# Kernel tuning notes

Hardware: AMD Instinct MI355X
Metric: run time of the kernel (lower is better)

## Reference

```python
import jax, jax.numpy as jnp
import numpy as np

N, E, G = 50000, 800000, 64
IN_C, HID, HEADS, OUT_C = 128, 64, 4, 10
NEG_SLOPE = 0.2
EPS = 1e-16


def gat_conv(x, src, dst, W, a_src, a_dst, bias, heads, out_ch):
    # x: [N, F_in]; W: [F_in, heads*out_ch]; a_*: [heads, out_ch]; bias: [heads*out_ch]
    n = x.shape[0]
    h = (x @ W).reshape(n, heads, out_ch)                     # [N, H, C]
    alpha_src = jnp.einsum('nhc,hc->nh', h, a_src)            # [N, H]
    alpha_dst = jnp.einsum('nhc,hc->nh', h, a_dst)            # [N, H]
    e = jax.nn.leaky_relu(alpha_src[src] + alpha_dst[dst], NEG_SLOPE)  # [E, H]
    # segment softmax over incoming edges of each destination node
    m = jax.ops.segment_max(e, dst, num_segments=n)
    ex = jnp.exp(e - m[dst])
    denom = jax.ops.segment_sum(ex, dst, num_segments=n)
    alpha = ex / (denom[dst] + EPS)                           # [E, H]
    msg = h[src] * alpha[:, :, None]                          # [E, H, C]
    out = jax.ops.segment_sum(msg, dst, num_segments=n)       # [N, H, C]
    return out.reshape(n, heads * out_ch) + bias


def setup_inputs() -> dict:
    key = jax.random.key(0)
    ks = jax.random.split(key, 16)
    s = 0.1
    inp = {
        'x': jax.random.normal(ks[0], (N, IN_C), dtype=jnp.float32),
        'edge_index': jax.random.randint(ks[1], (2, E), 0, N, dtype=jnp.int64)
            if jax.config.jax_enable_x64 else jax.random.randint(ks[1], (2, E), 0, N).astype(jnp.int32),
        'batch': jnp.sort(jax.random.randint(ks[2], (N,), 0, G).astype(jnp.int32)),
        'W1': s * jax.random.normal(ks[3], (IN_C, HEADS * HID), dtype=jnp.float32),
        'as1': s * jax.random.normal(ks[4], (HEADS, HID), dtype=jnp.float32),
        'ad1': s * jax.random.normal(ks[5], (HEADS, HID), dtype=jnp.float32),
        'b1': jnp.zeros((HEADS * HID,), jnp.float32),
        'W2': s * jax.random.normal(ks[6], (HEADS * HID, HEADS * HID), dtype=jnp.float32),
        'as2': s * jax.random.normal(ks[7], (HEADS, HID), dtype=jnp.float32),
        'ad2': s * jax.random.normal(ks[8], (HEADS, HID), dtype=jnp.float32),
        'b2': jnp.zeros((HEADS * HID,), jnp.float32),
        'W3': s * jax.random.normal(ks[9], (HEADS * HID, HID), dtype=jnp.float32),
        'as3': s * jax.random.normal(ks[10], (1, HID), dtype=jnp.float32),
        'ad3': s * jax.random.normal(ks[11], (1, HID), dtype=jnp.float32),
        'b3': jnp.zeros((HID,), jnp.float32),
        'Wc': s * jax.random.normal(ks[12], (HID, OUT_C), dtype=jnp.float32),
        'bc': jnp.zeros((OUT_C,), jnp.float32),
    }
    return inp


def reference(x, edge_index, batch, W1, as1, ad1, b1, W2, as2, ad2, b2,
              W3, as3, ad3, b3, Wc, bc):
    n = x.shape[0]
    loop = jnp.arange(n, dtype=edge_index.dtype)
    src = jnp.concatenate([edge_index[0], loop])  # add self-loops (PyG default)
    dst = jnp.concatenate([edge_index[1], loop])

    h = gat_conv(x, src, dst, W1, as1, ad1, b1, HEADS, HID)
    h = jax.nn.elu(h)
    h = gat_conv(h, src, dst, W2, as2, ad2, b2, HEADS, HID)
    h = jax.nn.elu(h)
    h = gat_conv(h, src, dst, W3, as3, ad3, b3, 1, HID)

    # global mean pool over graphs
    sums = jax.ops.segment_sum(h, batch, num_segments=G)            # [G, HID]
    counts = jax.ops.segment_sum(jnp.ones((n,), h.dtype), batch, num_segments=G)
    pooled = sums / jnp.maximum(counts, 1.0)[:, None]

    logits = pooled @ Wc + bc                                       # [G, OUT_C]
    return logits
```

## Files before the change

kernel.cpp:

```cpp
#include <hip/hip_runtime.h>

#define NEG_SLOPE 0.2f
#define EPSV 1e-16f

typedef unsigned short ushort_t;
typedef unsigned char uchar_t;
typedef __attribute__((ext_vector_type(8))) short bf16x8;
typedef __attribute__((ext_vector_type(4))) float f32x4;
typedef __attribute__((ext_vector_type(2))) float f32x2;

__device__ __forceinline__ ushort_t f2bf(float f) {
    union { float f; unsigned u; } v; v.f = f;
    unsigned r = v.u + 0x7FFFu + ((v.u >> 16) & 1u);
    return (ushort_t)(r >> 16);
}
__device__ __forceinline__ float bf2f(ushort_t u) {
    union { unsigned u; float f; } v; v.u = ((unsigned)u) << 16;
    return v.f;
}
__device__ __forceinline__ uchar_t f2fp8(float f) {
    int p = __builtin_amdgcn_cvt_pk_fp8_f32(f, 0.f, 0, false);
    return (uchar_t)(p & 0xff);
}

__global__ __launch_bounds__(256)
void count_kernel(const int* __restrict__ ei, int* __restrict__ deg, int E, int n) {
    int i = blockIdx.x * blockDim.x + threadIdx.x;
    int M = E + n;
    if (i >= M) return;
    int d = (i < E) ? ei[E + i] : (i - E);
    atomicAdd(&deg[d], 1);
}

__global__ __launch_bounds__(1024)
void scan1_kernel(const int* __restrict__ deg, int* __restrict__ indptr,
                  int* __restrict__ bsum, int n) {
    __shared__ int wsum[16];
    const int t = threadIdx.x;
    const int lane = t & 63;
    const int w = t >> 6;
    const int i = blockIdx.x * 1024 + t;
    int v = (i < n) ? deg[i] : 0;
    int s = v;
    #pragma unroll
    for (int off = 1; off < 64; off <<= 1) {
        int u = __shfl_up(s, off);
        if (lane >= off) s += u;
    }
    if (lane == 63) wsum[w] = s;
    __syncthreads();
    if (t < 16) {
        int ws_ = wsum[t];
        #pragma unroll
        for (int off = 1; off < 16; off <<= 1) {
            int u = __shfl_up(ws_, off);
            if (t >= off) ws_ += u;
        }
        wsum[t] = ws_;
    }
    __syncthreads();
    int woff = (w > 0) ? wsum[w - 1] : 0;
    if (i < n) indptr[i + 1] = woff + s;
    if (t == 0) bsum[blockIdx.x] = wsum[15];
}

__global__ __launch_bounds__(1024)
void scan3_kernel(int* __restrict__ indptr, int* __restrict__ cursor,
                  const int* __restrict__ bsum, int nb, int n) {
    __shared__ int boff_s;
    const int t = threadIdx.x;
    if (t < 64) {
        int v = (t < nb) ? bsum[t] : 0;
        int s = v;
        #pragma unroll
        for (int off = 1; off < 64; off <<= 1) {
            int u = __shfl_up(s, off);
            if (t >= off) s += u;
        }
        if (t == (int)blockIdx.x) boff_s = s - v;
    }
    __syncthreads();
    const int boff = boff_s;
    int i = blockIdx.x * 1024 + t;
    if (i < n) {
        int val = indptr[i + 1] + boff;
        indptr[i + 1] = val;
        cursor[i + 1] = val;
    }
    if (i == 0) { indptr[0] = 0; cursor[0] = 0; }
}

__global__ __launch_bounds__(256)
void scatter_kernel(const int* __restrict__ ei, int* __restrict__ cursor,
                    int* __restrict__ csr_src, int* __restrict__ csr_dst, int E, int n) {
    int i = blockIdx.x * blockDim.x + threadIdx.x;
    int M = E + n;
    if (i >= M) return;
    int s, d;
    if (i < E) { s = ei[i]; d = ei[E + i]; }
    else       { s = i - E; d = i - E; }
    int pos = atomicAdd(&cursor[d], 1);
    csr_src[pos] = s;
    csr_dst[pos] = d;
}

__global__ __launch_bounds__(256)
void prep_kernel(const float* __restrict__ x, ushort_t* __restrict__ xb, int nx4,
                 const float* __restrict__ W1, ushort_t* __restrict__ Wt1,
                 const float* __restrict__ W2, ushort_t* __restrict__ Wt2,
                 const float* __restrict__ W3, ushort_t* __restrict__ Wt3,
                 int K1, int* __restrict__ deg, int n) {
    long idx = (long)blockIdx.x * 256 + threadIdx.x;
    if (idx < nx4) {
        float4 v = *reinterpret_cast<const float4*>(&x[idx * 4]);
        ushort4 o;
        o.x = f2bf(v.x); o.y = f2bf(v.y); o.z = f2bf(v.z); o.w = f2bf(v.w);
        *reinterpret_cast<ushort4*>(&xb[idx * 4]) = o;
        return;
    }
    idx -= nx4;
    if (idx < (long)K1 * 256) {
        int c = (int)(idx % 256), k = (int)(idx / 256);
        Wt1[(long)c * K1 + k] = f2bf(W1[idx]);
        return;
    }
    idx -= (long)K1 * 256;
    if (idx < 256 * 256) {
        int c = (int)(idx % 256), k = (int)(idx / 256);
        Wt2[(long)c * 256 + k] = f2bf(W2[idx]);
        return;
    }
    idx -= 256 * 256;
    if (idx < 256 * 64) {
        int c = (int)(idx % 64), k = (int)(idx / 64);
        Wt3[(long)c * 256 + k] = f2bf(W3[idx]);
        return;
    }
    idx -= 256 * 64;
    if (idx < n) deg[idx] = 0;
}

template<int NC>
__global__ __launch_bounds__(256)
void mfma_gemm_alpha_kernel(const ushort_t* __restrict__ A, const ushort_t* __restrict__ Wt,
                            uchar_t* __restrict__ C,
                            const float* __restrict__ a_src, const float* __restrict__ a_dst,
                            float* __restrict__ asrc, float* __restrict__ adst,
                            int M, int K, int N, int H) {
    constexpr int TBN = NC * 64;
    constexpr int MI  = (NC == 2) ? 4 : 2;
    __shared__ ushort_t As[128][40];
    __shared__ ushort_t Ws[TBN][40];
    const int tid  = threadIdx.x;
    const int w    = tid >> 6;
    const int lane = tid & 63;
    const int l15  = lane & 15;
    const int l4   = lane >> 4;
    const int row0 = blockIdx.x * 128;
    const int col0 = blockIdx.y * TBN;
    const int rbase = (NC == 2) ? (w & 1) * 64 : w * 32;
    const int cbase = (NC == 2) ? (w >> 1) * 64 : 0;

    f32x4 acc[MI][4];
    #pragma unroll
    for (int mi = 0; mi < MI; ++mi)
        #pragma unroll
        for (int ni = 0; ni < 4; ++ni)
            acc[mi][ni] = (f32x4){0.f, 0.f, 0.f, 0.f};

    for (int k0 = 0; k0 < K; k0 += 32) {
        #pragma unroll
        for (int it = 0; it < 2; ++it) {
            int idx = tid + it * 256;
            int r = idx >> 2, seg = idx & 3;
            int gr = row0 + r;
            uint4 v = make_uint4(0u, 0u, 0u, 0u);
            if (gr < M)
                v = *reinterpret_cast<const uint4*>(&A[(long)gr * K + k0 + seg * 8]);
            *reinterpret_cast<uint4*>(&As[r][seg * 8]) = v;
        }
        #pragma unroll
        for (int it = 0; it < NC; ++it) {
            int idx = tid + it * 256;
            int r = idx >> 2, seg = idx & 3;
            uint4 v = *reinterpret_cast<const uint4*>(&Wt[(long)(col0 + r) * K + k0 + seg * 8]);
            *reinterpret_cast<uint4*>(&Ws[r][seg * 8]) = v;
        }
        __syncthreads();
        bf16x8 af[MI], bfv[4];
        #pragma unroll
        for (int mi = 0; mi < MI; ++mi)
            af[mi] = *reinterpret_cast<const bf16x8*>(&As[rbase + mi * 16 + l15][8 * l4]);
        #pragma unroll
        for (int ni = 0; ni < 4; ++ni)
            bfv[ni] = *reinterpret_cast<const bf16x8*>(&Ws[cbase + ni * 16 + l15][8 * l4]);
        #pragma unroll
        for (int mi = 0; mi < MI; ++mi)
            #pragma unroll
            for (int ni = 0; ni < 4; ++ni)
                acc[mi][ni] = __builtin_amdgcn_mfma_f32_16x16x32_bf16(
                    af[mi], bfv[ni], acc[mi][ni], 0, 0, 0);
        __syncthreads();
    }

    #pragma unroll
    for (int mi = 0; mi < MI; ++mi)
        #pragma unroll
        for (int reg = 0; reg < 4; ++reg) {
            int gr = row0 + rbase + mi * 16 + l4 * 4 + reg;
            if (gr < M) {
                #pragma unroll
                for (int ni = 0; ni < 4; ++ni)
                    C[(long)gr * N + col0 + cbase + ni * 16 + l15] = f2fp8(acc[mi][ni][reg]);
            }
        }

    const int hd = (col0 + cbase) >> 6;
    float aS[4], aD[4];
    #pragma unroll
    for (int ni = 0; ni < 4; ++ni) {
        aS[ni] = a_src[hd * 64 + ni * 16 + l15];
        aD[ni] = a_dst[hd * 64 + ni * 16 + l15];
    }
    #pragma unroll
    for (int mi = 0; mi < MI; ++mi)
        #pragma unroll
        for (int reg = 0; reg < 4; ++reg) {
            float s = 0.f, d = 0.f;
            #pragma unroll
            for (int ni = 0; ni < 4; ++ni) {
                s += acc[mi][ni][reg] * aS[ni];
                d += acc[mi][ni][reg] * aD[ni];
            }
            #pragma unroll
            for (int off = 1; off < 16; off <<= 1) {
                s += __shfl_xor(s, off);
                d += __shfl_xor(d, off);
            }
            int gr = row0 + rbase + mi * 16 + l4 * 4 + reg;
            if (l15 == 0 && gr < M) {
                asrc[gr * H + hd] = s;
                adst[gr * H + hd] = d;
            }
        }
}

__global__ __launch_bounds__(256)
void edgeexp4_kernel(const int* __restrict__ csr_src, const int* __restrict__ csr_dst,
                     const float4* __restrict__ asrc4, const float4* __restrict__ adst4,
                     float4* __restrict__ ex4, int M) {
    int i = blockIdx.x * blockDim.x + threadIdx.x;
    if (i >= M) return;
    int s = csr_src[i], d = csr_dst[i];
    float4 a = asrc4[s];
    float4 b = adst4[d];
    float ex_, ey_, ez_, ew_;
    float e;
    e = a.x + b.x; e = e > 0.f ? e : NEG_SLOPE * e; ex_ = __expf(e);
    e = a.y + b.y; e = e > 0.f ? e : NEG_SLOPE * e; ey_ = __expf(e);
    e = a.z + b.z; e = e > 0.f ? e : NEG_SLOPE * e; ez_ = __expf(e);
    e = a.w + b.w; e = e > 0.f ? e : NEG_SLOPE * e; ew_ = __expf(e);
    ex4[i] = make_float4(ex_, ey_, ez_, ew_);
}

__global__ __launch_bounds__(256)
void edgeexp1_kernel(const int* __restrict__ csr_src, const int* __restrict__ csr_dst,
                     const float* __restrict__ asrc, const float* __restrict__ adst,
                     float* __restrict__ ex1, int M) {
    int i = blockIdx.x * blockDim.x + threadIdx.x;
    if (i >= M) return;
    float e = asrc[csr_src[i]] + adst[csr_dst[i]];
    e = e > 0.f ? e : NEG_SLOPE * e;
    ex1[i] = __expf(e);
}

__global__ __launch_bounds__(256)
void aggregate4_kernel(const uchar_t* __restrict__ h, const float* __restrict__ ex4,
                       const int* __restrict__ indptr, const int* __restrict__ csr_src,
                       const float* __restrict__ bias, ushort_t* __restrict__ out,
                       int n, int apply_elu) {
    const int node = (blockIdx.x * blockDim.x + threadIdx.x) >> 6;
    const int lane = threadIdx.x & 63;
    if (node >= n) return;
    const int hd  = lane >> 4;
    const int beg = indptr[node], end = indptr[node + 1];
    const int cnt = end - beg;
    const uchar_t* __restrict__ hrow = h + 4 * lane;
    const float* __restrict__ exh = ex4 + 4 * (long)beg + hd;

    float sum_ex = 0.f;
    float ax = 0.f, ay = 0.f, az = 0.f, aw = 0.f;
    int i = 0;
    for (; i + 8 <= cnt; i += 8) {
        int s[8];
        float ee[8];
        unsigned v[8];
        #pragma unroll
        for (int u = 0; u < 8; ++u) s[u] = csr_src[beg + i + u];
        #pragma unroll
        for (int u = 0; u < 8; ++u) ee[u] = exh[(long)(i + u) * 4];
        #pragma unroll
        for (int u = 0; u < 8; ++u)
            v[u] = *reinterpret_cast<const unsigned*>(hrow + ((long)s[u] << 8));
        #pragma unroll
        for (int u = 0; u < 8; ++u) {
            f32x2 lo = __builtin_amdgcn_cvt_pk_f32_fp8((int)v[u], false);
            f32x2 hi = __builtin_amdgcn_cvt_pk_f32_fp8((int)v[u], true);
            sum_ex += ee[u];
            ax += ee[u] * lo[0];
            ay += ee[u] * lo[1];
            az += ee[u] * hi[0];
            aw += ee[u] * hi[1];
        }
    }
    for (; i < cnt; ++i) {
        int s = csr_src[beg + i];
        float ee = exh[(long)i * 4];
        unsigned v = *reinterpret_cast<const unsigned*>(hrow + ((long)s << 8));
        f32x2 lo = __builtin_amdgcn_cvt_pk_f32_fp8((int)v, false);
        f32x2 hi = __builtin_amdgcn_cvt_pk_f32_fp8((int)v, true);
        sum_ex += ee;
        ax += ee * lo[0]; ay += ee * lo[1];
        az += ee * hi[0]; aw += ee * hi[1];
    }
    const float inv = 1.f / (sum_ex + EPSV);
    float4 b4 = *reinterpret_cast<const float4*>(bias + 4 * lane);
    float ox = ax * inv + b4.x;
    float oy = ay * inv + b4.y;
    float oz = az * inv + b4.z;
    float ow = aw * inv + b4.w;
    if (apply_elu) {
        ox = ox > 0.f ? ox : expm1f(ox);
        oy = oy > 0.f ? oy : expm1f(oy);
        oz = oz > 0.f ? oz : expm1f(oz);
        ow = ow > 0.f ? ow : expm1f(ow);
    }
    ushort4 o4;
    o4.x = f2bf(ox); o4.y = f2bf(oy); o4.z = f2bf(oz); o4.w = f2bf(ow);
    *reinterpret_cast<ushort4*>(out + (long)node * 256 + 4 * lane) = o4;
}

__global__ __launch_bounds__(256)
void aggregate_kernel(const uchar_t* __restrict__ h, const float* __restrict__ ex1,
                      const int* __restrict__ indptr, const int* __restrict__ csr_src,
                      const float* __restrict__ bias, ushort_t* __restrict__ out,
                      int n, int apply_elu) {
    const int node = (blockIdx.x * blockDim.x + threadIdx.x) >> 6;
    const int lane = threadIdx.x & 63;
    if (node >= n) return;
    const int beg = indptr[node], end = indptr[node + 1];
    const int cnt = end - beg;
    const uchar_t* __restrict__ hh = h + lane;

    float sum_ex = 0.f, acc = 0.f;
    int i = 0;
    for (; i + 8 <= cnt; i += 8) {
        int s[8];
        float ee[8];
        uchar_t b[8];
        #pragma unroll
        for (int u = 0; u < 8; ++u) s[u] = csr_src[beg + i + u];
        #pragma unroll
        for (int u = 0; u < 8; ++u) ee[u] = ex1[beg + i + u];
        #pragma unroll
        for (int u = 0; u < 8; ++u) b[u] = hh[(long)s[u] << 6];
        #pragma unroll
        for (int u = 0; u < 8; ++u) {
            f32x2 r = __builtin_amdgcn_cvt_pk_f32_fp8((int)b[u], false);
            sum_ex += ee[u];
            acc += ee[u] * r[0];
        }
    }
    for (; i < cnt; ++i) {
        int s = csr_src[beg + i];
        float ee = ex1[beg + i];
        f32x2 r = __builtin_amdgcn_cvt_pk_f32_fp8((int)hh[(long)s << 6], false);
        sum_ex += ee;
        acc += ee * r[0];
    }
    float o = acc / (sum_ex + EPSV) + bias[lane];
    if (apply_elu) o = o > 0.f ? o : expm1f(o);
    out[(long)node * 64 + lane] = f2bf(o);
}

constexpr int POOL_CHUNK = 128;

__global__ __launch_bounds__(64)
void pool_kernel(const ushort_t* __restrict__ h, const int* __restrict__ batch,
                 float* __restrict__ sums, int* __restrict__ counts, int n) {
    int lane = threadIdx.x;
    int start = blockIdx.x * POOL_CHUNK;
    if (start >= n) return;
    int end = min(start + POOL_CHUNK, n);
    int gcur = batch[start];
    float acc = 0.f;
    int run = 0;
    for (int i = start; i < end; ++i) {
        int g = batch[i];
        if (g != gcur) {
            atomicAdd(&sums[gcur * 64 + lane], acc);
            if (lane == 0) atomicAdd(&counts[gcur], run);
            acc = 0.f; run = 0; gcur = g;
        }
        acc += bf2f(h[(long)i * 64 + lane]);
        ++run;
    }
    atomicAdd(&sums[gcur * 64 + lane], acc);
    if (lane == 0) atomicAdd(&counts[gcur], run);
}

__global__ void classify_kernel(const float* __restrict__ sums, const int* __restrict__ counts,
                                const float* __restrict__ Wc, const float* __restrict__ bc,
                                float* __restrict__ out, int G) {
    int t = threadIdx.x;
    if (t >= G * 10) return;
    int g = t / 10, o = t - g * 10;
    int c_ = counts[g];
    float inv = 1.f / (float)(c_ > 1 ? c_ : 1);
    float acc = bc[o];
    for (int c = 0; c < 64; ++c)
        acc += sums[g * 64 + c] * inv * Wc[c * 10 + o];
    out[t] = acc;
}

extern "C" void kernel_launch(void* const* d_in, const int* in_sizes, int n_in,
                              void* d_out, int out_size, void* d_ws, size_t ws_size,
                              hipStream_t stream) {
    const float* x   = (const float*)d_in[0];
    const int*   ei  = (const int*)d_in[1];
    const int*   bat = (const int*)d_in[2];
    const float* W1  = (const float*)d_in[3];
    const float* as1 = (const float*)d_in[4];
    const float* ad1 = (const float*)d_in[5];
    const float* b1  = (const float*)d_in[6];
    const float* W2  = (const float*)d_in[7];
    const float* as2 = (const float*)d_in[8];
    const float* ad2 = (const float*)d_in[9];
    const float* b2  = (const float*)d_in[10];
    const float* W3  = (const float*)d_in[11];
    const float* as3 = (const float*)d_in[12];
    const float* ad3 = (const float*)d_in[13];
    const float* b3  = (const float*)d_in[14];
    const float* Wc  = (const float*)d_in[15];
    const float* bc  = (const float*)d_in[16];
    float* out = (float*)d_out;

    const int N = in_sizes[2];
    const int E = in_sizes[1] / 2;
    const int M = E + N;
    const int IN_C = in_sizes[0] / N;
    const int G = out_size / 10;

    char* p = (char*)d_ws;
    auto carve = [&](size_t bytes) -> void* {
        void* r = (void*)p;
        p += (bytes + 255) & ~(size_t)255;
        return r;
    };
    uchar_t*  hA  = (uchar_t*)carve((size_t)N * 256);
    ushort_t* hB  = (ushort_t*)carve((size_t)N * 256 * 2);
    size_t xb_ex_bytes = (size_t)M * 16;
    size_t xb_need = (size_t)N * IN_C * 2;
    if (xb_need > xb_ex_bytes) xb_ex_bytes = xb_need;
    ushort_t* xb  = (ushort_t*)carve(xb_ex_bytes);
    float*    ex  = (float*)xb;
    ushort_t* Wt1 = (ushort_t*)carve((size_t)256 * IN_C * 2);
    ushort_t* Wt2 = (ushort_t*)carve((size_t)256 * 256 * 2);
    ushort_t* Wt3 = (ushort_t*)carve((size_t)64 * 256 * 2);
    float* asrc = (float*)carve((size_t)N * 4 * 4);
    float* adst = (float*)carve((size_t)N * 4 * 4);
    float* sums = (float*)carve((size_t)G * 64 * 4 + (size_t)G * 4);
    int*   cnts = (int*)(sums + (size_t)G * 64);
    int*   deg  = (int*)carve((size_t)N * 4);
    int*   iptr = (int*)carve((size_t)(N + 1) * 4);
    int*   csr  = (int*)carve((size_t)M * 4);
    int*   csrd = (int*)carve((size_t)M * 4);
    int*   bsum = (int*)carve(256 * 4);
    (void)ws_size; (void)n_in;

    const int NB = (N + 1023) / 1024;
    const int MB = (M + 255) / 256;
    const int AGB = (N + 3) / 4;

    {
        long nx4 = (long)N * IN_C / 4;
        long total = nx4 + (long)IN_C * 256 + 256 * 256 + 256 * 64 + N;
        prep_kernel<<<(int)((total + 255) / 256), 256, 0, stream>>>(
            x, xb, (int)nx4, W1, Wt1, W2, Wt2, W3, Wt3, IN_C, deg, N);
    }

    count_kernel<<<MB, 256, 0, stream>>>(ei, deg, E, N);
    scan1_kernel<<<NB, 1024, 0, stream>>>(deg, iptr, bsum, N);
    scan3_kernel<<<NB, 1024, 0, stream>>>(iptr, deg, bsum, NB, N);
    scatter_kernel<<<MB, 256, 0, stream>>>(ei, deg, csr, csrd, E, N);

    {
        dim3 grid((N + 127) / 128, 2);
        mfma_gemm_alpha_kernel<2><<<grid, 256, 0, stream>>>(xb, Wt1, hA, as1, ad1,
                                                            asrc, adst, N, IN_C, 256, 4);
    }
    edgeexp4_kernel<<<MB, 256, 0, stream>>>(csr, csrd, (const float4*)asrc,
                                            (const float4*)adst, (float4*)ex, M);
    aggregate4_kernel<<<AGB, 256, 0, stream>>>(hA, ex, iptr, csr, b1, hB, N, 1);

    {
        dim3 grid((N + 127) / 128, 2);
        mfma_gemm_alpha_kernel<2><<<grid, 256, 0, stream>>>(hB, Wt2, hA, as2, ad2,
                                                            asrc, adst, N, 256, 256, 4);
    }
    edgeexp4_kernel<<<MB, 256, 0, stream>>>(csr, csrd, (const float4*)asrc,
                                            (const float4*)adst, (float4*)ex, M);
    aggregate4_kernel<<<AGB, 256, 0, stream>>>(hA, ex, iptr, csr, b2, hB, N, 1);

    {
        dim3 grid((N + 127) / 128, 1);
        mfma_gemm_alpha_kernel<1><<<grid, 256, 0, stream>>>(hB, Wt3, hA, as3, ad3,
                                                            asrc, adst, N, 256, 64, 1);
    }
    edgeexp1_kernel<<<MB, 256, 0, stream>>>(csr, csrd, asrc, adst, ex, M);
    aggregate_kernel<<<AGB, 256, 0, stream>>>(hA, ex, iptr, csr, b3, hB, N, 0);

    hipMemsetAsync(sums, 0, (size_t)G * 64 * 4 + (size_t)G * 4, stream);
    pool_kernel<<<(N + POOL_CHUNK - 1) / POOL_CHUNK, 64, 0, stream>>>(hB, bat, sums, cnts, N);
    classify_kernel<<<1, 640, 0, stream>>>(sums, cnts, Wc, bc, out, G);
}
```

Measured before the change: 454.2 us.

## Drop CSR dst array, make edge-exp kernels node-centric, fold pool zeroing into prep

The edge-exp kernels now walk the CSR per destination node, one wavefront per node, with the adst value loaded once. This removes the stored csr_dst array and its writes in scatter and reads in three edge passes. The pool accumulator memset is folded into the prep kernel, saving one launch. The cost is load imbalance across nodes of different degree, and idle lanes when degree is low (about 17 edges per node here, so 16-lane groups per head often run a second, mostly empty iteration).

```diff
diff --git a/kernel.cpp b/kernel.cpp
--- a/kernel.cpp
+++ b/kernel.cpp
@@ -92,7 +92,7 @@
 
 __global__ __launch_bounds__(256)
 void scatter_kernel(const int* __restrict__ ei, int* __restrict__ cursor,
-                    int* __restrict__ csr_src, int* __restrict__ csr_dst, int E, int n) {
+                    int* __restrict__ csr_src, int E, int n) {
     int i = blockIdx.x * blockDim.x + threadIdx.x;
     int M = E + n;
     if (i >= M) return;
@@ -101,7 +101,6 @@
     else       { s = i - E; d = i - E; }
     int pos = atomicAdd(&cursor[d], 1);
     csr_src[pos] = s;
-    csr_dst[pos] = d;
 }
 
 __global__ __launch_bounds__(256)
@@ -109,7 +108,8 @@
                  const float* __restrict__ W1, ushort_t* __restrict__ Wt1,
                  const float* __restrict__ W2, ushort_t* __restrict__ Wt2,
                  const float* __restrict__ W3, ushort_t* __restrict__ Wt3,
-                 int K1, int* __restrict__ deg, int n) {
+                 int K1, int* __restrict__ deg, int n,
+                 int* __restrict__ poolz, int gz) {
     long idx = (long)blockIdx.x * 256 + threadIdx.x;
     if (idx < nx4) {
         float4 v = *reinterpret_cast<const float4*>(&x[idx * 4]);
@@ -137,7 +137,9 @@
         return;
     }
     idx -= 256 * 64;
-    if (idx < n) deg[idx] = 0;
+    if (idx < n) { deg[idx] = 0; return; }
+    idx -= n;
+    if (idx < gz) poolz[idx] = 0;
 }
 
 template<int NC>
@@ -246,32 +248,38 @@
 }
 
 __global__ __launch_bounds__(256)
-void edgeexp4_kernel(const int* __restrict__ csr_src, const int* __restrict__ csr_dst,
-                     const float4* __restrict__ asrc4, const float4* __restrict__ adst4,
-                     float4* __restrict__ ex4, int M) {
-    int i = blockIdx.x * blockDim.x + threadIdx.x;
-    if (i >= M) return;
-    int s = csr_src[i], d = csr_dst[i];
-    float4 a = asrc4[s];
-    float4 b = adst4[d];
-    float ex_, ey_, ez_, ew_;
-    float e;
-    e = a.x + b.x; e = e > 0.f ? e : NEG_SLOPE * e; ex_ = __expf(e);
-    e = a.y + b.y; e = e > 0.f ? e : NEG_SLOPE * e; ey_ = __expf(e);
-    e = a.z + b.z; e = e > 0.f ? e : NEG_SLOPE * e; ez_ = __expf(e);
-    e = a.w + b.w; e = e > 0.f ? e : NEG_SLOPE * e; ew_ = __expf(e);
-    ex4[i] = make_float4(ex_, ey_, ez_, ew_);
-}
-
-__global__ __launch_bounds__(256)
-void edgeexp1_kernel(const int* __restrict__ csr_src, const int* __restrict__ csr_dst,
+void edgeexp4_kernel(const int* __restrict__ indptr, const int* __restrict__ csr_src,
                      const float* __restrict__ asrc, const float* __restrict__ adst,
-                     float* __restrict__ ex1, int M) {
-    int i = blockIdx.x * blockDim.x + threadIdx.x;
-    if (i >= M) return;
-    float e = asrc[csr_src[i]] + adst[csr_dst[i]];
-    e = e > 0.f ? e : NEG_SLOPE * e;
-    ex1[i] = __expf(e);
+                     float* __restrict__ ex4, int n) {
+    const int node = (blockIdx.x * blockDim.x + threadIdx.x) >> 6;
+    const int lane = threadIdx.x & 63;
+    if (node >= n) return;
+    const int hd = lane >> 4;
+    const int eidx = lane & 15;
+    const int beg = indptr[node], end = indptr[node + 1];
+    const float ad = adst[node * 4 + hd];
+    for (int i = beg + eidx; i < end; i += 16) {
+        int s = csr_src[i];
+        float e = asrc[s * 4 + hd] + ad;
+        e = e > 0.f ? e : NEG_SLOPE * e;
+        ex4[(long)i * 4 + hd] = __expf(e);
+    }
+}
+
+__global__ __launch_bounds__(256)
+void edgeexp1_kernel(const int* __restrict__ indptr, const int* __restrict__ csr_src,
+                     const float* __restrict__ asrc, const float* __restrict__ adst,
+                     float* __restrict__ ex1, int n) {
+    const int node = (blockIdx.x * blockDim.x + threadIdx.x) >> 6;
+    const int lane = threadIdx.x & 63;
+    if (node >= n) return;
+    const int beg = indptr[node], end = indptr[node + 1];
+    const float ad = adst[node];
+    for (int i = beg + lane; i < end; i += 64) {
+        float e = asrc[csr_src[i]] + ad;
+        e = e > 0.f ? e : NEG_SLOPE * e;
+        ex1[i] = __expf(e);
+    }
 }
 
 __global__ __launch_bounds__(256)
@@ -474,7 +482,6 @@
     int*   deg  = (int*)carve((size_t)N * 4);
     int*   iptr = (int*)carve((size_t)(N + 1) * 4);
     int*   csr  = (int*)carve((size_t)M * 4);
-    int*   csrd = (int*)carve((size_t)M * 4);
     int*   bsum = (int*)carve(256 * 4);
     (void)ws_size; (void)n_in;
 
@@ -484,23 +491,23 @@
 
     {
         long nx4 = (long)N * IN_C / 4;
-        long total = nx4 + (long)IN_C * 256 + 256 * 256 + 256 * 64 + N;
+        int gz = G * 65;
+        long total = nx4 + (long)IN_C * 256 + 256 * 256 + 256 * 64 + N + gz;
         prep_kernel<<<(int)((total + 255) / 256), 256, 0, stream>>>(
-            x, xb, (int)nx4, W1, Wt1, W2, Wt2, W3, Wt3, IN_C, deg, N);
+            x, xb, (int)nx4, W1, Wt1, W2, Wt2, W3, Wt3, IN_C, deg, N, (int*)sums, gz);
     }
 
     count_kernel<<<MB, 256, 0, stream>>>(ei, deg, E, N);
     scan1_kernel<<<NB, 1024, 0, stream>>>(deg, iptr, bsum, N);
     scan3_kernel<<<NB, 1024, 0, stream>>>(iptr, deg, bsum, NB, N);
-    scatter_kernel<<<MB, 256, 0, stream>>>(ei, deg, csr, csrd, E, N);
+    scatter_kernel<<<MB, 256, 0, stream>>>(ei, deg, csr, E, N);
 
     {
         dim3 grid((N + 127) / 128, 2);
         mfma_gemm_alpha_kernel<2><<<grid, 256, 0, stream>>>(xb, Wt1, hA, as1, ad1,
                                                             asrc, adst, N, IN_C, 256, 4);
     }
-    edgeexp4_kernel<<<MB, 256, 0, stream>>>(csr, csrd, (const float4*)asrc,
-                                            (const float4*)adst, (float4*)ex, M);
+    edgeexp4_kernel<<<AGB, 256, 0, stream>>>(iptr, csr, asrc, adst, ex, N);
     aggregate4_kernel<<<AGB, 256, 0, stream>>>(hA, ex, iptr, csr, b1, hB, N, 1);
 
     {
@@ -508,8 +515,7 @@
         mfma_gemm_alpha_kernel<2><<<grid, 256, 0, stream>>>(hB, Wt2, hA, as2, ad2,
                                                             asrc, adst, N, 256, 256, 4);
     }
-    edgeexp4_kernel<<<MB, 256, 0, stream>>>(csr, csrd, (const float4*)asrc,
-                                            (const float4*)adst, (float4*)ex, M);
+    edgeexp4_kernel<<<AGB, 256, 0, stream>>>(iptr, csr, asrc, adst, ex, N);
     aggregate4_kernel<<<AGB, 256, 0, stream>>>(hA, ex, iptr, csr, b2, hB, N, 1);
 
     {
@@ -517,10 +523,9 @@
         mfma_gemm_alpha_kernel<1><<<grid, 256, 0, stream>>>(hB, Wt3, hA, as3, ad3,
                                                             asrc, adst, N, 256, 64, 1);
     }
-    edgeexp1_kernel<<<MB, 256, 0, stream>>>(csr, csrd, asrc, adst, ex, M);
+    edgeexp1_kernel<<<AGB, 256, 0, stream>>>(iptr, csr, asrc, adst, ex, N);
     aggregate_kernel<<<AGB, 256, 0, stream>>>(hA, ex, iptr, csr, b3, hB, N, 0);
 
-    hipMemsetAsync(sums, 0, (size_t)G * 64 * 4 + (size_t)G * 4, stream);
     pool_kernel<<<(N + POOL_CHUNK - 1) / POOL_CHUNK, 64, 0, stream>>>(hB, bat, sums, cnts, N);
     classify_kernel<<<1, 640, 0, stream>>>(sums, cnts, Wc, bc, out, G);
 }
```

Result: slower. 473.6 us (+4.3%).

## Replicate degree counters and pack CSR src/dst into 16-bit pairs

Applied to the files above, without the earlier changes.

Degree counting and scatter use 8 replicated counter arrays selected by block index to spread atomic contention, with the scan computing per-replica cursor offsets. The CSR source and destination are packed into one 32-bit word (16 bits each), halving index reads in the edge kernels. The pool-sum memset is folded into the prep kernel. Packing assumes node count fits in 16 bits and the replicas add scan work and memory.

```diff
diff --git a/kernel.cpp b/kernel.cpp
--- a/kernel.cpp
+++ b/kernel.cpp
@@ -24,23 +24,27 @@
 }
 
 __global__ __launch_bounds__(256)
-void count_kernel(const int* __restrict__ ei, int* __restrict__ deg, int E, int n) {
+void count_kernel(const int* __restrict__ ei, int* __restrict__ deg8, int E, int n) {
     int i = blockIdx.x * blockDim.x + threadIdx.x;
     int M = E + n;
     if (i >= M) return;
     int d = (i < E) ? ei[E + i] : (i - E);
-    atomicAdd(&deg[d], 1);
+    atomicAdd(&deg8[(blockIdx.x & 7) * n + d], 1);
 }
 
 __global__ __launch_bounds__(1024)
-void scan1_kernel(const int* __restrict__ deg, int* __restrict__ indptr,
+void scan1_kernel(const int* __restrict__ deg8, int* __restrict__ indptr,
                   int* __restrict__ bsum, int n) {
     __shared__ int wsum[16];
     const int t = threadIdx.x;
     const int lane = t & 63;
     const int w = t >> 6;
     const int i = blockIdx.x * 1024 + t;
-    int v = (i < n) ? deg[i] : 0;
+    int v = 0;
+    if (i < n) {
+        #pragma unroll
+        for (int j = 0; j < 8; ++j) v += deg8[j * n + i];
+    }
     int s = v;
     #pragma unroll
     for (int off = 1; off < 64; off <<= 1) {
@@ -65,10 +69,13 @@
 }
 
 __global__ __launch_bounds__(1024)
-void scan3_kernel(int* __restrict__ indptr, int* __restrict__ cursor,
+void scan3_kernel(int* __restrict__ indptr, int* __restrict__ deg8,
                   const int* __restrict__ bsum, int nb, int n) {
     __shared__ int boff_s;
     const int t = threadIdx.x;
+    const int i = blockIdx.x * 1024 + t;
+    int lv1 = (i < n) ? indptr[i + 1] : 0;
+    int lv0 = (i < n && t > 0) ? indptr[i] : 0;
     if (t < 64) {
         int v = (t < nb) ? bsum[t] : 0;
         int s = v;
@@ -81,27 +88,30 @@
     }
     __syncthreads();
     const int boff = boff_s;
-    int i = blockIdx.x * 1024 + t;
     if (i < n) {
-        int val = indptr[i + 1] + boff;
-        indptr[i + 1] = val;
-        cursor[i + 1] = val;
-    }
-    if (i == 0) { indptr[0] = 0; cursor[0] = 0; }
-}
-
-__global__ __launch_bounds__(256)
-void scatter_kernel(const int* __restrict__ ei, int* __restrict__ cursor,
-                    int* __restrict__ csr_src, int* __restrict__ csr_dst, int E, int n) {
+        indptr[i + 1] = lv1 + boff;
+        int running = (t == 0) ? boff : lv0 + boff;
+        #pragma unroll
+        for (int j = 0; j < 8; ++j) {
+            int c = deg8[j * n + i];
+            deg8[j * n + i] = running;
+            running += c;
+        }
+    }
+    if (i == 0) indptr[0] = 0;
+}
+
+__global__ __launch_bounds__(256)
+void scatter_kernel(const int* __restrict__ ei, int* __restrict__ cursor8,
+                    unsigned* __restrict__ csrp, int E, int n) {
     int i = blockIdx.x * blockDim.x + threadIdx.x;
     int M = E + n;
     if (i >= M) return;
     int s, d;
     if (i < E) { s = ei[i]; d = ei[E + i]; }
     else       { s = i - E; d = i - E; }
-    int pos = atomicAdd(&cursor[d], 1);
-    csr_src[pos] = s;
-    csr_dst[pos] = d;
+    int pos = atomicAdd(&cursor8[(blockIdx.x & 7) * n + d], 1);
+    csrp[pos] = (unsigned)s | ((unsigned)d << 16);
 }
 
 __global__ __launch_bounds__(256)
@@ -109,7 +119,8 @@
                  const float* __restrict__ W1, ushort_t* __restrict__ Wt1,
                  const float* __restrict__ W2, ushort_t* __restrict__ Wt2,
                  const float* __restrict__ W3, ushort_t* __restrict__ Wt3,
-                 int K1, int* __restrict__ deg, int n) {
+                 int K1, int* __restrict__ deg8, int n8,
+                 int* __restrict__ poolz, int gz) {
     long idx = (long)blockIdx.x * 256 + threadIdx.x;
     if (idx < nx4) {
         float4 v = *reinterpret_cast<const float4*>(&x[idx * 4]);
@@ -137,7 +148,9 @@
         return;
     }
     idx -= 256 * 64;
-    if (idx < n) deg[idx] = 0;
+    if (idx < n8) { deg8[idx] = 0; return; }
+    idx -= n8;
+    if (idx < gz) poolz[idx] = 0;
 }
 
 template<int NC>
@@ -246,16 +259,16 @@
 }
 
 __global__ __launch_bounds__(256)
-void edgeexp4_kernel(const int* __restrict__ csr_src, const int* __restrict__ csr_dst,
+void edgeexp4_kernel(const unsigned* __restrict__ csrp,
                      const float4* __restrict__ asrc4, const float4* __restrict__ adst4,
                      float4* __restrict__ ex4, int M) {
     int i = blockIdx.x * blockDim.x + threadIdx.x;
     if (i >= M) return;
-    int s = csr_src[i], d = csr_dst[i];
+    unsigned v = csrp[i];
+    int s = (int)(v & 0xffffu), d = (int)(v >> 16);
     float4 a = asrc4[s];
     float4 b = adst4[d];
-    float ex_, ey_, ez_, ew_;
-    float e;
+    float e, ex_, ey_, ez_, ew_;
     e = a.x + b.x; e = e > 0.f ? e : NEG_SLOPE * e; ex_ = __expf(e);
     e = a.y + b.y; e = e > 0.f ? e : NEG_SLOPE * e; ey_ = __expf(e);
     e = a.z + b.z; e = e > 0.f ? e : NEG_SLOPE * e; ez_ = __expf(e);
@@ -264,19 +277,20 @@
 }
 
 __global__ __launch_bounds__(256)
-void edgeexp1_kernel(const int* __restrict__ csr_src, const int* __restrict__ csr_dst,
+void edgeexp1_kernel(const unsigned* __restrict__ csrp,
                      const float* __restrict__ asrc, const float* __restrict__ adst,
                      float* __restrict__ ex1, int M) {
     int i = blockIdx.x * blockDim.x + threadIdx.x;
     if (i >= M) return;
-    float e = asrc[csr_src[i]] + adst[csr_dst[i]];
+    unsigned v = csrp[i];
+    float e = asrc[v & 0xffffu] + adst[v >> 16];
     e = e > 0.f ? e : NEG_SLOPE * e;
     ex1[i] = __expf(e);
 }
 
 __global__ __launch_bounds__(256)
 void aggregate4_kernel(const uchar_t* __restrict__ h, const float* __restrict__ ex4,
-                       const int* __restrict__ indptr, const int* __restrict__ csr_src,
+                       const int* __restrict__ indptr, const unsigned* __restrict__ csrp,
                        const float* __restrict__ bias, ushort_t* __restrict__ out,
                        int n, int apply_elu) {
     const int node = (blockIdx.x * blockDim.x + threadIdx.x) >> 6;
@@ -292,16 +306,16 @@
     float ax = 0.f, ay = 0.f, az = 0.f, aw = 0.f;
     int i = 0;
     for (; i + 8 <= cnt; i += 8) {
-        int s[8];
+        long s[8];
         float ee[8];
         unsigned v[8];
         #pragma unroll
-        for (int u = 0; u < 8; ++u) s[u] = csr_src[beg + i + u];
+        for (int u = 0; u < 8; ++u) s[u] = (long)(csrp[beg + i + u] & 0xffffu);
         #pragma unroll
         for (int u = 0; u < 8; ++u) ee[u] = exh[(long)(i + u) * 4];
         #pragma unroll
         for (int u = 0; u < 8; ++u)
-            v[u] = *reinterpret_cast<const unsigned*>(hrow + ((long)s[u] << 8));
+            v[u] = *reinterpret_cast<const unsigned*>(hrow + (s[u] << 8));
         #pragma unroll
         for (int u = 0; u < 8; ++u) {
             f32x2 lo = __builtin_amdgcn_cvt_pk_f32_fp8((int)v[u], false);
@@ -314,9 +328,9 @@
         }
     }
     for (; i < cnt; ++i) {
-        int s = csr_src[beg + i];
+        long s = (long)(csrp[beg + i] & 0xffffu);
         float ee = exh[(long)i * 4];
-        unsigned v = *reinterpret_cast<const unsigned*>(hrow + ((long)s << 8));
+        unsigned v = *reinterpret_cast<const unsigned*>(hrow + (s << 8));
         f32x2 lo = __builtin_amdgcn_cvt_pk_f32_fp8((int)v, false);
         f32x2 hi = __builtin_amdgcn_cvt_pk_f32_fp8((int)v, true);
         sum_ex += ee;
@@ -342,7 +356,7 @@
 
 __global__ __launch_bounds__(256)
 void aggregate_kernel(const uchar_t* __restrict__ h, const float* __restrict__ ex1,
-                      const int* __restrict__ indptr, const int* __restrict__ csr_src,
+                      const int* __restrict__ indptr, const unsigned* __restrict__ csrp,
                       const float* __restrict__ bias, ushort_t* __restrict__ out,
                       int n, int apply_elu) {
     const int node = (blockIdx.x * blockDim.x + threadIdx.x) >> 6;
@@ -355,15 +369,15 @@
     float sum_ex = 0.f, acc = 0.f;
     int i = 0;
     for (; i + 8 <= cnt; i += 8) {
-        int s[8];
+        long s[8];
         float ee[8];
         uchar_t b[8];
         #pragma unroll
-        for (int u = 0; u < 8; ++u) s[u] = csr_src[beg + i + u];
+        for (int u = 0; u < 8; ++u) s[u] = (long)(csrp[beg + i + u] & 0xffffu);
         #pragma unroll
         for (int u = 0; u < 8; ++u) ee[u] = ex1[beg + i + u];
         #pragma unroll
-        for (int u = 0; u < 8; ++u) b[u] = hh[(long)s[u] << 6];
+        for (int u = 0; u < 8; ++u) b[u] = hh[s[u] << 6];
         #pragma unroll
         for (int u = 0; u < 8; ++u) {
             f32x2 r = __builtin_amdgcn_cvt_pk_f32_fp8((int)b[u], false);
@@ -372,9 +386,9 @@
         }
     }
     for (; i < cnt; ++i) {
-        int s = csr_src[beg + i];
+        long s = (long)(csrp[beg + i] & 0xffffu);
         float ee = ex1[beg + i];
-        f32x2 r = __builtin_amdgcn_cvt_pk_f32_fp8((int)hh[(long)s << 6], false);
+        f32x2 r = __builtin_amdgcn_cvt_pk_f32_fp8((int)hh[s << 6], false);
         sum_ex += ee;
         acc += ee * r[0];
     }
@@ -471,10 +485,9 @@
     float* adst = (float*)carve((size_t)N * 4 * 4);
     float* sums = (float*)carve((size_t)G * 64 * 4 + (size_t)G * 4);
     int*   cnts = (int*)(sums + (size_t)G * 64);
-    int*   deg  = (int*)carve((size_t)N * 4);
+    int*   deg8 = (int*)carve((size_t)8 * N * 4);
     int*   iptr = (int*)carve((size_t)(N + 1) * 4);
-    int*   csr  = (int*)carve((size_t)M * 4);
-    int*   csrd = (int*)carve((size_t)M * 4);
+    unsigned* csrp = (unsigned*)carve((size_t)M * 4);
     int*   bsum = (int*)carve(256 * 4);
     (void)ws_size; (void)n_in;
 
@@ -484,43 +497,43 @@
 
     {
         long nx4 = (long)N * IN_C / 4;
-        long total = nx4 + (long)IN_C * 256 + 256 * 256 + 256 * 64 + N;
+        int gz = G * 65;
+        long total = nx4 + (long)IN_C * 256 + 256 * 256 + 256 * 64 + 8L * N + gz;
         prep_kernel<<<(int)((total + 255) / 256), 256, 0, stream>>>(
-            x, xb, (int)nx4, W1, Wt1, W2, Wt2, W3, Wt3, IN_C, deg, N);
-    }
-
-    count_kernel<<<MB, 256, 0, stream>>>(ei, deg, E, N);
-    scan1_kernel<<<NB, 1024, 0, stream>>>(deg, iptr, bsum, N);
-    scan3_kernel<<<NB, 1024, 0, stream>>>(iptr, deg, bsum, NB, N);
-    scatter_kernel<<<MB, 256, 0, stream>>>(ei, deg, csr, csrd, E, N);
+            x, xb, (int)nx4, W1, Wt1, W2, Wt2, W3, Wt3, IN_C, deg8, 8 * N, (int*)sums, gz);
+    }
+
+    count_kernel<<<MB, 256, 0, stream>>>(ei, deg8, E, N);
+    scan1_kernel<<<NB, 1024, 0, stream>>>(deg8, iptr, bsum, N);
+    scan3_kernel<<<NB, 1024, 0, stream>>>(iptr, deg8, bsum, NB, N);
+    scatter_kernel<<<MB, 256, 0, stream>>>(ei, deg8, csrp, E, N);
 
     {
         dim3 grid((N + 127) / 128, 2);
         mfma_gemm_alpha_kernel<2><<<grid, 256, 0, stream>>>(xb, Wt1, hA, as1, ad1,
                                                             asrc, adst, N, IN_C, 256, 4);
     }
-    edgeexp4_kernel<<<MB, 256, 0, stream>>>(csr, csrd, (const float4*)asrc,
+    edgeexp4_kernel<<<MB, 256, 0, stream>>>(csrp, (const float4*)asrc,
                                             (const float4*)adst, (float4*)ex, M);
-    aggregate4_kernel<<<AGB, 256, 0, stream>>>(hA, ex, iptr, csr, b1, hB, N, 1);
+    aggregate4_kernel<<<AGB, 256, 0, stream>>>(hA, ex, iptr, csrp, b1, hB, N, 1);
 
     {
         dim3 grid((N + 127) / 128, 2);
         mfma_gemm_alpha_kernel<2><<<grid, 256, 0, stream>>>(hB, Wt2, hA, as2, ad2,
                                                             asrc, adst, N, 256, 256, 4);
     }
-    edgeexp4_kernel<<<MB, 256, 0, stream>>>(csr, csrd, (const float4*)asrc,
+    edgeexp4_kernel<<<MB, 256, 0, stream>>>(csrp, (const float4*)asrc,
                                             (const float4*)adst, (float4*)ex, M);
-    aggregate4_kernel<<<AGB, 256, 0, stream>>>(hA, ex, iptr, csr, b2, hB, N, 1);
+    aggregate4_kernel<<<AGB, 256, 0, stream>>>(hA, ex, iptr, csrp, b2, hB, N, 1);
 
     {
         dim3 grid((N + 127) / 128, 1);
         mfma_gemm_alpha_kernel<1><<<grid, 256, 0, stream>>>(hB, Wt3, hA, as3, ad3,
                                                             asrc, adst, N, 256, 64, 1);
     }
-    edgeexp1_kernel<<<MB, 256, 0, stream>>>(csr, csrd, asrc, adst, ex, M);
-    aggregate_kernel<<<AGB, 256, 0, stream>>>(hA, ex, iptr, csr, b3, hB, N, 0);
-
-    hipMemsetAsync(sums, 0, (size_t)G * 64 * 4 + (size_t)G * 4, stream);
+    edgeexp1_kernel<<<MB, 256, 0, stream>>>(csrp, asrc, adst, ex, M);
+    aggregate_kernel<<<AGB, 256, 0, stream>>>(hA, ex, iptr, csrp, b3, hB, N, 0);
+
     pool_kernel<<<(N + POOL_CHUNK - 1) / POOL_CHUNK, 64, 0, stream>>>(hB, bat, sums, cnts, N);
     classify_kernel<<<1, 640, 0, stream>>>(sums, cnts, Wc, bc, out, G);
 }
```

Result: no change. 448.1 us (-1.4%).
